# Kernel tuning notes

Hardware: AMD Instinct MI355X
Metric: run time of the kernel (lower is better)

The kernel has to match this reference:

```python
import jax, jax.numpy as jnp
import numpy as np

B, S, E, H = 4, 4096, 1024, 16
D = E // H  # head_dim = 64


def _xavier(key, out_f, in_f):
    lim = float(np.sqrt(6.0 / (in_f + out_f)))
    return jax.random.uniform(key, (out_f, in_f), jnp.float32, -lim, lim)


def setup_inputs() -> dict:
    key = jax.random.key(0)
    ks = jax.random.split(key, 9)
    x = jax.random.normal(ks[0], (B, S, E), jnp.float32)
    Wq = _xavier(ks[1], E, E)
    Wk = _xavier(ks[2], E, E)
    Wv = _xavier(ks[3], E, E)
    Wo = _xavier(ks[4], E, E)
    bq = jnp.zeros((E,), jnp.float32)
    bk = jnp.zeros((E,), jnp.float32)
    bv = jnp.zeros((E,), jnp.float32)
    bo = jnp.zeros((E,), jnp.float32)
    return {"x": x, "Wq": Wq, "bq": bq, "Wk": Wk, "bk": bk,
            "Wv": Wv, "bv": bv, "Wo": Wo, "bo": bo}


def _feature_map(t):
    # elu(t) + 1 (positive feature map)
    return jax.nn.elu(t) + 1.0


def reference(x, Wq, bq, Wk, bk, Wv, bv, Wo, bo):
    b, s, _ = x.shape
    # projections (torch Linear: y = x @ W.T + b), reshape to [b, s, h, d]
    Q = (x @ Wq.T + bq).reshape(b, s, H, D)
    K = (x @ Wk.T + bk).reshape(b, s, H, D)
    V = (x @ Wv.T + bv).reshape(b, s, H, D)
    Q = _feature_map(Q)
    K = _feature_map(K)
    # KV summary: [b, h, d, e]
    KV = jnp.einsum('bshd,bshe->bhde', K, V)
    K_sum = K.sum(axis=1)  # [b, h, d]
    Z = 1.0 / (jnp.einsum('bshd,bhd->bsh', Q, K_sum) + 1e-6)  # [b, s, h]
    out = jnp.einsum('bshd,bhde,bsh->bshe', Q, KV, Z)  # [b, s, h, e]
    out = out.reshape(b, s, E)
    out = out @ Wo.T + bo
    return out
```

## Files before the change

### kernel.cpp

```cpp
#include <hip/hip_runtime.h>
#include <math.h>

#define BB 4
#define SS 4096
#define EE 1024
#define HH 16
#define DD 64
#define MM (BB*SS)

typedef _Float16 f16x8 __attribute__((ext_vector_type(8)));
typedef _Float16 f16x4 __attribute__((ext_vector_type(4)));
typedef float    f32x4 __attribute__((ext_vector_type(4)));

typedef __attribute__((address_space(3))) void lds_void;
typedef __attribute__((address_space(1))) void gm_void;

__device__ __forceinline__ void gload16(const void* g, void* l) {
  __builtin_amdgcn_global_load_lds((gm_void*)g, (lds_void*)l, 16, 0, 0);
}

__global__ __launch_bounds__(256) void conv_all_kernel(const float* __restrict__ x,
                                                       const float* __restrict__ Wq,
                                                       const float* __restrict__ Wk,
                                                       const float* __restrict__ Wv,
                                                       const float* __restrict__ Wo,
                                                       _Float16* __restrict__ xh,
                                                       _Float16* __restrict__ wqkv,
                                                       _Float16* __restrict__ woh) {
  const int nx4 = (MM * EE) / 4;
  const int per = (EE * EE) / 4;
  const int ntot = nx4 + 4 * per;
  int i = blockIdx.x * blockDim.x + threadIdx.x;
  int stride = gridDim.x * blockDim.x;
  for (; i < ntot; i += stride) {
    const float* src;
    _Float16* dst;
    int off;
    if (i < nx4) {
      src = x; dst = xh; off = i;
    } else {
      int j = i - nx4;
      int seg = j / per; off = j - seg * per;
      src = (seg == 0) ? Wq : (seg == 1) ? Wk : (seg == 2) ? Wv : Wo;
      dst = (seg < 3) ? (wqkv + (size_t)seg * EE * EE) : woh;
    }
    f32x4 v = *(const f32x4*)&src[(size_t)off * 4];
    f16x4 h;
    h[0] = (_Float16)v[0]; h[1] = (_Float16)v[1];
    h[2] = (_Float16)v[2]; h[3] = (_Float16)v[3];
    *(f16x4*)&dst[(size_t)off * 4] = h;
  }
}


#define SCB() __builtin_amdgcn_sched_barrier(0)
#define VMW0 asm volatile("s_waitcnt vmcnt(0)" ::: "memory")
#define BARR do { SCB(); __builtin_amdgcn_s_barrier(); SCB(); } while (0)

#define STAGE_A(t, g) gload16(Ag + ((size_t)(g) << 15) + (size_t)(t) * 64,   \
                              LdsA + (((t) & 1) << 14) + (((wv << 2) + (g)) << 10))
#define STAGE_B(t, g) gload16(Bg + ((size_t)(g) << 15) + (size_t)(t) * 64,   \
                              LdsB + (((t) & 1) << 13) + (((wv << 1) + (g)) << 10))
#define STG6(t) do { STAGE_A(t, 0); STAGE_A(t, 1); STAGE_A(t, 2);            \
                     STAGE_B(t, 0); STAGE_B(t, 1); STAGE_A(t, 3); } while (0)

#define RD_A(par, mf) (*(const f16x8*)(LdsA + ((par) << 14) + ((wr8 + (mf)) << 10) + lof))
#define RD_B(par, nf) (*(const f16x8*)(LdsB + ((par) << 13) + ((wc4 + (nf)) << 10) + lof))

template <int EPI>
__global__ __launch_bounds__(256, 3) void gemm256(const _Float16* __restrict__ A,
                                                  const _Float16* __restrict__ Bw,
                                                  const float* __restrict__ bias0,
                                                  const float* __restrict__ bias1,
                                                  const float* __restrict__ bias2,
                                                  _Float16* __restrict__ O0,
                                                  _Float16* __restrict__ O1,
                                                  _Float16* __restrict__ O2,
                                                  float* __restrict__ OF) {
  __shared__ __align__(16) char lds[49152];
  char* LdsA = lds;
  char* LdsB = lds + 32768;

  const int tid  = threadIdx.x;
  const int lane = tid & 63;
  const int wv   = tid >> 6;
  const int wr   = wv >> 1;
  const int wc   = wv & 1;
  const int wr8  = wr << 3;
  const int wc4  = wc << 2;

  constexpr int NXT = (EPI == 0) ? 24 : 8;
  const int q = (int)gridDim.x >> 3;
  const int bid = (int)blockIdx.x;
  const int sid = (bid & 7) * q + (bid >> 3);
  const int mbase = (sid / NXT) << 8;
  const int nbase = (sid % NXT) << 7;

  const int lof = ((lane & 15) << 6) + (((lane >> 4) ^ ((lane >> 1) & 3)) << 4);
  const int plane = ((lane >> 2) << 11) + (((lane & 3) ^ ((lane >> 3) & 3)) << 4);

  const char* Ag = (const char*)A + ((size_t)(mbase + (wv << 6)) << 11) + plane;
  const char* Bg = (const char*)Bw + ((size_t)(nbase + (wv << 5)) << 11) + plane;

  f32x4 acc[8][4] = {};

  STG6(0);
  VMW0; BARR;

#pragma unroll 1
  for (int t = 0; t < 32; ++t) {
    const int par = t & 1;
    if (t < 31) STG6(t + 1);
    f16x8 fB0 = RD_B(par, 0), fB1 = RD_B(par, 1);
    f16x8 fB2 = RD_B(par, 2), fB3 = RD_B(par, 3);
    __builtin_amdgcn_s_setprio(1);
#pragma unroll
    for (int mf = 0; mf < 8; mf++) {
      if (mf == 4) SCB();
      f16x8 fA = RD_A(par, mf);
      acc[mf][0] = __builtin_amdgcn_mfma_f32_16x16x32_f16(fA, fB0, acc[mf][0], 0, 0, 0);
      acc[mf][1] = __builtin_amdgcn_mfma_f32_16x16x32_f16(fA, fB1, acc[mf][1], 0, 0, 0);
      acc[mf][2] = __builtin_amdgcn_mfma_f32_16x16x32_f16(fA, fB2, acc[mf][2], 0, 0, 0);
      acc[mf][3] = __builtin_amdgcn_mfma_f32_16x16x32_f16(fA, fB3, acc[mf][3], 0, 0, 0);
    }
    __builtin_amdgcn_s_setprio(0);
    if (t < 31) { VMW0; BARR; }
  }

  const int rl = (lane >> 4) << 2;
  const int cl = lane & 15;
  const int rb = mbase + (wr << 7);
  if (EPI == 0) {
    const int which = nbase >> 10;
    const float* bias = (which == 0) ? bias0 : (which == 1) ? bias1 : bias2;
    _Float16* O = (which == 0) ? O0 : (which == 1) ? O1 : O2;
    const int cb = (nbase & 1023) + (wc << 6);
#pragma unroll
    for (int mf = 0; mf < 8; mf++) {
      const int gm = rb + (mf << 4) + rl;
#pragma unroll
      for (int nf = 0; nf < 4; nf++) {
        const int gc = cb + (nf << 4) + cl;
        const float bz = bias[gc];
#pragma unroll
        for (int j = 0; j < 4; j++) {
          float v = acc[mf][nf][j] + bz;
          if (which < 2) v = (v > 0.f) ? (v + 1.f) : expf(v);
          O[(size_t)(gm + j) * EE + gc] = (_Float16)v;
        }
      }
    }
  } else {
    const int cb = nbase + (wc << 6);
#pragma unroll
    for (int mf = 0; mf < 8; mf++) {
      const int gm = rb + (mf << 4) + rl;
#pragma unroll
      for (int nf = 0; nf < 4; nf++) {
        const int gc = cb + (nf << 4) + cl;
        const float bz = bias0[gc];
#pragma unroll
        for (int j = 0; j < 4; j++)
          OF[(size_t)(gm + j) * EE + gc] = acc[mf][nf][j] + bz;
      }
    }
  }
}

#undef RD_A
#undef RD_B
#undef STG6
#undef STAGE_A
#undef STAGE_B

__global__ __launch_bounds__(256) void kv_partial_kernel(const _Float16* __restrict__ Kh,
                                                         const _Float16* __restrict__ Vh,
                                                         float* __restrict__ kvpart,
                                                         float* __restrict__ ksump) {
  __shared__ __align__(16) _Float16 Ks[64 * 64];
  __shared__ __align__(16) _Float16 Vs[64 * 64];
  const int tid = threadIdx.x;
  const int wv = tid >> 6;
  const int bh = blockIdx.x;
  const int chunk = blockIdx.y;
  const int b = bh >> 4, h = bh & 15;
  const int td = tid >> 4, te = tid & 15;
  const int d0 = td * 4, e0 = te * 4;

  float kv[4][4] = {};
  float ks4[4] = {0.f, 0.f, 0.f, 0.f};

  for (int sub = 0; sub < 4; sub++) {
    const int s0 = chunk * 256 + sub * 64;
    __syncthreads();
    {
      const int g0 = tid, g1 = tid + 256;
      gload16((const char*)Kh + ((size_t)(b * SS + s0 + (g0 >> 3)) * EE + h * DD) * 2 + (g0 & 7) * 16,
              (char*)Ks + wv * 1024);
      gload16((const char*)Kh + ((size_t)(b * SS + s0 + (g1 >> 3)) * EE + h * DD) * 2 + (g1 & 7) * 16,
              (char*)Ks + 4096 + wv * 1024);
      gload16((const char*)Vh + ((size_t)(b * SS + s0 + (g0 >> 3)) * EE + h * DD) * 2 + (g0 & 7) * 16,
              (char*)Vs + wv * 1024);
      gload16((const char*)Vh + ((size_t)(b * SS + s0 + (g1 >> 3)) * EE + h * DD) * 2 + (g1 & 7) * 16,
              (char*)Vs + 4096 + wv * 1024);
    }
    __syncthreads();
#pragma unroll 8
    for (int s = 0; s < 64; s++) {
      f16x4 kk = *(const f16x4*)&Ks[s * 64 + d0];
      f16x4 vv = *(const f16x4*)&Vs[s * 64 + e0];
      float kf[4], vf[4];
#pragma unroll
      for (int i = 0; i < 4; i++) { kf[i] = (float)kk[i]; vf[i] = (float)vv[i]; }
#pragma unroll
      for (int i = 0; i < 4; i++)
#pragma unroll
        for (int j = 0; j < 4; j++) kv[i][j] += kf[i] * vf[j];
      if (te == 0) {
#pragma unroll
        for (int i = 0; i < 4; i++) ks4[i] += kf[i];
      }
    }
  }
  const size_t base = ((size_t)chunk * 64 + bh) * 4096;
#pragma unroll
  for (int i = 0; i < 4; i++)
#pragma unroll
    for (int j = 0; j < 4; j++) kvpart[base + (size_t)(d0 + i) * 64 + e0 + j] = kv[i][j];
  if (te == 0) {
#pragma unroll
    for (int i = 0; i < 4; i++) ksump[((size_t)chunk * 64 + bh) * 64 + d0 + i] = ks4[i];
  }
}

__global__ __launch_bounds__(256) void kv_reduce_kernel(const float* __restrict__ kvpart,
                                                        const float* __restrict__ ksump,
                                                        _Float16* __restrict__ kvt,
                                                        float* __restrict__ ksum) {
  const int idx = blockIdx.x * 256 + threadIdx.x;
  if (blockIdx.x < 1024) {
    const int bh = idx >> 12;
    const int rem = idx & 4095;
    float s = 0.f;
#pragma unroll
    for (int c = 0; c < 16; c++) s += kvpart[((size_t)c * 64 + bh) * 4096 + rem];
    const int d = rem >> 6, e = rem & 63;
    kvt[(size_t)bh * 4096 + e * 64 + d] = (_Float16)s;
  } else {
    const int i2 = idx - 1024 * 256;
    const int bh = i2 >> 6, d = i2 & 63;
    float s = 0.f;
#pragma unroll
    for (int c = 0; c < 16; c++) s += ksump[((size_t)c * 64 + bh) * 64 + d];
    ksum[i2] = s;
  }
}

__global__ __launch_bounds__(256) void attn_kernel(const _Float16* __restrict__ Qh,
                                                   const _Float16* __restrict__ kvt,
                                                   const float* __restrict__ ksum,
                                                   _Float16* __restrict__ attn) {
  __shared__ __align__(16) _Float16 Qs[64 * 64];
  __shared__ __align__(16) _Float16 KVs[64 * 64];
  __shared__ float ks_lds[64];
  __shared__ float dpart[4][64];
  __shared__ float zr[64];
  const int tid = threadIdx.x;
  const int lane = tid & 63;
  const int wv = tid >> 6;
  const int stile = blockIdx.x;
  const int bh = blockIdx.y;
  const int b = bh >> 4, h = bh & 15;
  const int m0 = b * SS + stile * 64;

  {
    const int g0 = tid, g1 = tid + 256;
    gload16((const char*)Qh + ((size_t)(m0 + (g0 >> 3)) * EE + h * DD) * 2 + (g0 & 7) * 16,
            (char*)Qs + wv * 1024);
    gload16((const char*)Qh + ((size_t)(m0 + (g1 >> 3)) * EE + h * DD) * 2 + (g1 & 7) * 16,
            (char*)Qs + 4096 + wv * 1024);
    gload16((const char*)kvt + (size_t)bh * 8192 + (size_t)g0 * 16, (char*)KVs + wv * 1024);
    gload16((const char*)kvt + (size_t)bh * 8192 + (size_t)g1 * 16, (char*)KVs + 4096 + wv * 1024);
  }
  if (tid < 64) ks_lds[tid] = ksum[bh * 64 + tid];
  __syncthreads();

  {
    const int r = tid & 63, qd = tid >> 6;
    float p = 0.f;
#pragma unroll
    for (int i = 0; i < 16; i++) p += (float)Qs[r * 64 + qd * 16 + i] * ks_lds[qd * 16 + i];
    dpart[qd][r] = p;
  }
  __syncthreads();
  if (tid < 64) {
    float den = dpart[0][tid] + dpart[1][tid] + dpart[2][tid] + dpart[3][tid];
    zr[tid] = 1.f / (den + 1e-6f);
  }
  __syncthreads();

  f32x4 acc[4] = {};
  const int fr = lane & 15;
  const int kg = (lane >> 4) * 8;
#pragma unroll
  for (int kh = 0; kh < 2; kh++) {
    f16x8 a = *(const f16x8*)&Qs[(wv * 16 + fr) * 64 + kh * 32 + kg];
#pragma unroll
    for (int n = 0; n < 4; n++) {
      f16x8 b8 = *(const f16x8*)&KVs[(n * 16 + fr) * 64 + kh * 32 + kg];
      acc[n] = __builtin_amdgcn_mfma_f32_16x16x32_f16(a, b8, acc[n], 0, 0, 0);
    }
  }

  const int rl = (lane >> 4) * 4, cl = lane & 15;
#pragma unroll
  for (int n = 0; n < 4; n++)
#pragma unroll
    for (int j = 0; j < 4; j++) {
      const int r = wv * 16 + rl + j;
      float v = acc[n][j] * zr[r];
      attn[(size_t)(m0 + r) * EE + h * DD + n * 16 + cl] = (_Float16)v;
    }
}

extern "C" void kernel_launch(void* const* d_in, const int* in_sizes, int n_in,
                              void* d_out, int out_size, void* d_ws, size_t ws_size,
                              hipStream_t stream) {
  const float* x  = (const float*)d_in[0];
  const float* Wq = (const float*)d_in[1];
  const float* bq = (const float*)d_in[2];
  const float* Wk = (const float*)d_in[3];
  const float* bk = (const float*)d_in[4];
  const float* Wv = (const float*)d_in[5];
  const float* bv = (const float*)d_in[6];
  const float* Wo = (const float*)d_in[7];
  const float* bo = (const float*)d_in[8];
  float* out = (float*)d_out;

  char* ws = (char*)d_ws;
  size_t off = 0;
  auto alloc = [&](size_t bytes) -> char* {
    char* p = ws + off;
    off += (bytes + 255) & ~(size_t)255;
    return p;
  };
  _Float16* xh    = (_Float16*)alloc((size_t)MM * EE * 2);
  _Float16* wqkv  = (_Float16*)alloc((size_t)3 * EE * EE * 2);
  _Float16* woh   = (_Float16*)alloc((size_t)EE * EE * 2);
  _Float16* Qh    = (_Float16*)alloc((size_t)MM * EE * 2);
  _Float16* Kh    = (_Float16*)alloc((size_t)MM * EE * 2);
  _Float16* Vh    = (_Float16*)alloc((size_t)MM * EE * 2);
  float*    kvpart= (float*)alloc((size_t)16 * 64 * 4096 * 4);
  float*    ksump = (float*)alloc((size_t)16 * 64 * 64 * 4);
  _Float16* kvt   = (_Float16*)alloc((size_t)64 * 4096 * 2);
  float*    ksum  = (float*)alloc((size_t)64 * 64 * 4);
  _Float16* attn  = xh;

  (void)in_sizes; (void)n_in; (void)out_size; (void)ws_size;

  conv_all_kernel<<<2560, 256, 0, stream>>>(x, Wq, Wk, Wv, Wo, xh, wqkv, woh);
  gemm256<0><<<1536, 256, 0, stream>>>(xh, wqkv, bq, bk, bv, Qh, Kh, Vh, nullptr);
  kv_partial_kernel<<<dim3(64, 16), 256, 0, stream>>>(Kh, Vh, kvpart, ksump);
  kv_reduce_kernel<<<1040, 256, 0, stream>>>(kvpart, ksump, kvt, ksum);
  attn_kernel<<<dim3(64, 64), 256, 0, stream>>>(Qh, kvt, ksum, attn);
  gemm256<1><<<512, 256, 0, stream>>>(attn, woh, bo, nullptr, nullptr,
                                      nullptr, nullptr, nullptr, out);
}
```

Measured before the change: 261.8 us.

## Triple-buffer GEMM LDS staging with two tiles in flight

Changes the GEMM main loop from double to triple buffering in LDS. Two k-tiles are now prefetched, and each step waits with vmcnt(6) so only the older tile has to land, which hides more global-load latency. The loop is unrolled by three so buffer indices are compile-time constants. LDS grows from 48KB to 72KB and the occupancy hint drops from 3 to 2 blocks per CU, trading occupancy for deeper prefetch.

```diff
diff --git a/kernel.cpp b/kernel.cpp
--- a/kernel.cpp
+++ b/kernel.cpp
@@ -54,21 +54,40 @@
 
 
 #define SCB() __builtin_amdgcn_sched_barrier(0)
+#define VMW6 asm volatile("s_waitcnt vmcnt(6)" ::: "memory")
 #define VMW0 asm volatile("s_waitcnt vmcnt(0)" ::: "memory")
 #define BARR do { SCB(); __builtin_amdgcn_s_barrier(); SCB(); } while (0)
-
-#define STAGE_A(t, g) gload16(Ag + ((size_t)(g) << 15) + (size_t)(t) * 64,   \
-                              LdsA + (((t) & 1) << 14) + (((wv << 2) + (g)) << 10))
-#define STAGE_B(t, g) gload16(Bg + ((size_t)(g) << 15) + (size_t)(t) * 64,   \
-                              LdsB + (((t) & 1) << 13) + (((wv << 1) + (g)) << 10))
-#define STG6(t) do { STAGE_A(t, 0); STAGE_A(t, 1); STAGE_A(t, 2);            \
-                     STAGE_B(t, 0); STAGE_B(t, 1); STAGE_A(t, 3); } while (0)
-
-#define RD_A(par, mf) (*(const f16x8*)(LdsA + ((par) << 14) + ((wr8 + (mf)) << 10) + lof))
-#define RD_B(par, nf) (*(const f16x8*)(LdsB + ((par) << 13) + ((wc4 + (nf)) << 10) + lof))
+#define NOP_ do {} while (0)
+
+#define STAGE_A(t, g, bf) gload16(Ag + ((size_t)(g) << 15) + (size_t)(t) * 64, \
+                                  LdsA + (bf) * 16384 + (((wv << 2) + (g)) << 10))
+#define STAGE_B(t, g, bf) gload16(Bg + ((size_t)(g) << 15) + (size_t)(t) * 64, \
+                                  LdsB + (bf) * 8192 + (((wv << 1) + (g)) << 10))
+#define STG6(t, bf) do { STAGE_A(t, 0, bf); STAGE_A(t, 1, bf); STAGE_A(t, 2, bf); \
+                         STAGE_B(t, 0, bf); STAGE_B(t, 1, bf); STAGE_A(t, 3, bf); } while (0)
+
+#define RD_A(bf, mf) (*(const f16x8*)(LdsA + (bf) * 16384 + ((wr8 + (mf)) << 10) + lof))
+#define RD_B(bf, nf) (*(const f16x8*)(LdsB + (bf) * 8192 + ((wc4 + (nf)) << 10) + lof))
+
+#define TILE_(bf, STG, VW, BAR) do {                                         \
+    STG;                                                                     \
+    f16x8 fB0 = RD_B(bf, 0), fB1 = RD_B(bf, 1);                              \
+    f16x8 fB2 = RD_B(bf, 2), fB3 = RD_B(bf, 3);                              \
+    __builtin_amdgcn_s_setprio(1);                                           \
+    _Pragma("unroll") for (int mf = 0; mf < 8; mf++) {                       \
+      if (mf == 4) SCB();                                                    \
+      f16x8 fA = RD_A(bf, mf);                                               \
+      acc[mf][0] = __builtin_amdgcn_mfma_f32_16x16x32_f16(fA, fB0, acc[mf][0], 0, 0, 0); \
+      acc[mf][1] = __builtin_amdgcn_mfma_f32_16x16x32_f16(fA, fB1, acc[mf][1], 0, 0, 0); \
+      acc[mf][2] = __builtin_amdgcn_mfma_f32_16x16x32_f16(fA, fB2, acc[mf][2], 0, 0, 0); \
+      acc[mf][3] = __builtin_amdgcn_mfma_f32_16x16x32_f16(fA, fB3, acc[mf][3], 0, 0, 0); \
+    }                                                                        \
+    __builtin_amdgcn_s_setprio(0);                                           \
+    VW; BAR;                                                                 \
+  } while (0)
 
 template <int EPI>
-__global__ __launch_bounds__(256, 3) void gemm256(const _Float16* __restrict__ A,
+__global__ __launch_bounds__(256, 2) void gemm256(const _Float16* __restrict__ A,
                                                   const _Float16* __restrict__ Bw,
                                                   const float* __restrict__ bias0,
                                                   const float* __restrict__ bias1,
@@ -77,9 +96,9 @@
                                                   _Float16* __restrict__ O1,
                                                   _Float16* __restrict__ O2,
                                                   float* __restrict__ OF) {
-  __shared__ __align__(16) char lds[49152];
+  __shared__ __align__(16) char lds[73728];
   char* LdsA = lds;
-  char* LdsB = lds + 32768;
+  char* LdsB = lds + 49152;
 
   const int tid  = threadIdx.x;
   const int lane = tid & 63;
@@ -104,28 +123,18 @@
 
   f32x4 acc[8][4] = {};
 
-  STG6(0);
-  VMW0; BARR;
+  STG6(0, 0); STG6(1, 1);
+  VMW6; BARR;
 
 #pragma unroll 1
-  for (int t = 0; t < 32; ++t) {
-    const int par = t & 1;
-    if (t < 31) STG6(t + 1);
-    f16x8 fB0 = RD_B(par, 0), fB1 = RD_B(par, 1);
-    f16x8 fB2 = RD_B(par, 2), fB3 = RD_B(par, 3);
-    __builtin_amdgcn_s_setprio(1);
-#pragma unroll
-    for (int mf = 0; mf < 8; mf++) {
-      if (mf == 4) SCB();
-      f16x8 fA = RD_A(par, mf);
-      acc[mf][0] = __builtin_amdgcn_mfma_f32_16x16x32_f16(fA, fB0, acc[mf][0], 0, 0, 0);
-      acc[mf][1] = __builtin_amdgcn_mfma_f32_16x16x32_f16(fA, fB1, acc[mf][1], 0, 0, 0);
-      acc[mf][2] = __builtin_amdgcn_mfma_f32_16x16x32_f16(fA, fB2, acc[mf][2], 0, 0, 0);
-      acc[mf][3] = __builtin_amdgcn_mfma_f32_16x16x32_f16(fA, fB3, acc[mf][3], 0, 0, 0);
-    }
-    __builtin_amdgcn_s_setprio(0);
-    if (t < 31) { VMW0; BARR; }
-  }
+  for (int i = 0; i < 10; ++i) {
+    const int t = i * 3;
+    TILE_(0, STG6(t + 2, 2), VMW6, BARR);
+    TILE_(1, STG6(t + 3, 0), VMW6, BARR);
+    TILE_(2, STG6(t + 4, 1), VMW6, BARR);
+  }
+  TILE_(0, NOP_, VMW0, BARR);
+  TILE_(1, NOP_, NOP_, NOP_);
 
   const int rl = (lane >> 4) << 2;
   const int cl = lane & 15;
@@ -167,6 +176,7 @@
   }
 }
 
+#undef TILE_
 #undef RD_A
 #undef RD_B
 #undef STG6
```

Measured after the change: 265.1 us. Within noise of the previous version (+1.3%).

## Rework GEMM to 256x256 tiles with 8 waves and phased k-pipelining

Applied to the files above, without the earlier changes.

The GEMM kernel moves from 256x128 tiles with 4 waves and K-step 32 to 256x256 tiles with 8 waves, K-step 64 and a 128KB double-buffered LDS. Each K tile is split into four phases that interleave global-to-LDS prefetch of future tiles with MFMA work, using partial vmcnt waits instead of a full drain. The intent is higher arithmetic intensity per tile, fewer barrier stalls and better overlap of loads with compute. In exchange the kernel uses much more LDS per block, which lowers occupancy, and the barrier schedule is more complex.

```diff
diff --git a/kernel.cpp b/kernel.cpp
--- a/kernel.cpp
+++ b/kernel.cpp
@@ -53,22 +53,59 @@
 }
 
 
-#define SCB() __builtin_amdgcn_sched_barrier(0)
+#define VMW6 asm volatile("s_waitcnt vmcnt(6)" ::: "memory")
 #define VMW0 asm volatile("s_waitcnt vmcnt(0)" ::: "memory")
-#define BARR do { SCB(); __builtin_amdgcn_s_barrier(); SCB(); } while (0)
-
-#define STAGE_A(t, g) gload16(Ag + ((size_t)(g) << 15) + (size_t)(t) * 64,   \
-                              LdsA + (((t) & 1) << 14) + (((wv << 2) + (g)) << 10))
-#define STAGE_B(t, g) gload16(Bg + ((size_t)(g) << 15) + (size_t)(t) * 64,   \
-                              LdsB + (((t) & 1) << 13) + (((wv << 1) + (g)) << 10))
-#define STG6(t) do { STAGE_A(t, 0); STAGE_A(t, 1); STAGE_A(t, 2);            \
-                     STAGE_B(t, 0); STAGE_B(t, 1); STAGE_A(t, 3); } while (0)
-
-#define RD_A(par, mf) (*(const f16x8*)(LdsA + ((par) << 14) + ((wr8 + (mf)) << 10) + lof))
-#define RD_B(par, nf) (*(const f16x8*)(LdsB + ((par) << 13) + ((wc4 + (nf)) << 10) + lof))
+#define NOP_ do {} while (0)
+
+#define STA(t, h) do {                                                        \
+    const char* s_ = AgL + (size_t)(h) * 262144 + (size_t)(t) * 128;          \
+    char* d_ = LdsA + (((t) & 1) << 15) + ((h) << 14) + (wv << 10);           \
+    gload16(s_, d_); gload16(s_ + 131072, d_ + 8192);                         \
+  } while (0)
+#define STB(t, h) do {                                                        \
+    const char* s_ = BgL + (size_t)(h) * 262144 + (size_t)(t) * 128;          \
+    char* d_ = LdsB + (((t) & 1) << 15) + ((h) << 14) + (wv << 10);           \
+    gload16(s_, d_); gload16(s_ + 131072, d_ + 8192);                         \
+  } while (0)
+
+#define RA(bu, mf, ks) (*(const f16x8*)(LdsA + ((bu) << 15) + (wr << 14) +    \
+    ((mf) << 11) + frb + ((ks) ? so1 : so0)))
+#define RB(bu, nf, ks) (*(const f16x8*)(LdsB + ((bu) << 15) + ((wc >> 1) << 14) + \
+    ((((wc & 1) << 2) | (nf)) << 11) + frb + ((ks) ? so1 : so0)))
+
+#define PHASE(t, P, STG, VMC) do {                                            \
+    const int bu = (t) & 1;                                                   \
+    if ((P) == 0) {                                                           \
+      _Pragma("unroll") for (int nf = 0; nf < 4; nf++) {                      \
+        bfr[nf][0] = RB(bu, nf, 0); bfr[nf][1] = RB(bu, nf, 1);               \
+      }                                                                       \
+    }                                                                         \
+    f16x8 a00 = RA(bu, 2 * (P), 0),     a01 = RA(bu, 2 * (P), 1);             \
+    f16x8 a10 = RA(bu, 2 * (P) + 1, 0), a11 = RA(bu, 2 * (P) + 1, 1);         \
+    STG;                                                                      \
+    __builtin_amdgcn_s_barrier();                                             \
+    __builtin_amdgcn_s_setprio(1);                                            \
+    _Pragma("unroll") for (int nf = 0; nf < 4; nf++) {                        \
+      acc[2*(P)][nf]   = __builtin_amdgcn_mfma_f32_16x16x32_f16(a00, bfr[nf][0], acc[2*(P)][nf], 0, 0, 0);   \
+      acc[2*(P)][nf]   = __builtin_amdgcn_mfma_f32_16x16x32_f16(a01, bfr[nf][1], acc[2*(P)][nf], 0, 0, 0);   \
+      acc[2*(P)+1][nf] = __builtin_amdgcn_mfma_f32_16x16x32_f16(a10, bfr[nf][0], acc[2*(P)+1][nf], 0, 0, 0); \
+      acc[2*(P)+1][nf] = __builtin_amdgcn_mfma_f32_16x16x32_f16(a11, bfr[nf][1], acc[2*(P)+1][nf], 0, 0, 0); \
+    }                                                                         \
+    __builtin_amdgcn_s_setprio(0);                                            \
+    VMC;                                                                      \
+    __builtin_amdgcn_s_barrier();                                             \
+  } while (0)
+
+#define TILE(t, S1, S2, S3, S4, VMC) do {                                     \
+    PHASE(t, 0, S1, NOP_);                                                    \
+    PHASE(t, 1, S2, NOP_);                                                    \
+    PHASE(t, 2, S3, NOP_);                                                    \
+    PHASE(t, 3, S4, VMC);                                                     \
+    __builtin_amdgcn_sched_barrier(0);                                        \
+  } while (0)
 
 template <int EPI>
-__global__ __launch_bounds__(256, 3) void gemm256(const _Float16* __restrict__ A,
+__global__ __launch_bounds__(512, 2) void gemm256(const _Float16* __restrict__ A,
                                                   const _Float16* __restrict__ Bw,
                                                   const float* __restrict__ bias0,
                                                   const float* __restrict__ bias1,
@@ -77,55 +114,52 @@
                                                   _Float16* __restrict__ O1,
                                                   _Float16* __restrict__ O2,
                                                   float* __restrict__ OF) {
-  __shared__ __align__(16) char lds[49152];
+  __shared__ __align__(16) char lds[131072];
   char* LdsA = lds;
-  char* LdsB = lds + 32768;
+  char* LdsB = lds + 65536;
 
   const int tid  = threadIdx.x;
   const int lane = tid & 63;
   const int wv   = tid >> 6;
-  const int wr   = wv >> 1;
-  const int wc   = wv & 1;
-  const int wr8  = wr << 3;
-  const int wc4  = wc << 2;
-
-  constexpr int NXT = (EPI == 0) ? 24 : 8;
+  const int wr   = wv >> 2;
+  const int wc   = wv & 3;
+
+  constexpr int NX = (EPI == 0) ? 12 : 4;
   const int q = (int)gridDim.x >> 3;
   const int bid = (int)blockIdx.x;
   const int sid = (bid & 7) * q + (bid >> 3);
-  const int mbase = (sid / NXT) << 8;
-  const int nbase = (sid % NXT) << 7;
-
-  const int lof = ((lane & 15) << 6) + (((lane >> 4) ^ ((lane >> 1) & 3)) << 4);
-  const int plane = ((lane >> 2) << 11) + (((lane & 3) ^ ((lane >> 3) & 3)) << 4);
-
-  const char* Ag = (const char*)A + ((size_t)(mbase + (wv << 6)) << 11) + plane;
-  const char* Bg = (const char*)Bw + ((size_t)(nbase + (wv << 5)) << 11) + plane;
+  const int mbase = (sid / NX) << 8;
+  const int nbase = (sid % NX) << 8;
+
+  const int fr  = lane & 15;
+  const int kg  = lane >> 4;
+  const int frb = fr << 7;
+  const int so0 = ((kg ^ (fr & 7)) << 4);
+  const int so1 = (((4 | kg) ^ (fr & 7)) << 4);
+  const int srcsl = (((lane & 7) ^ (lane >> 3)) << 4);
+
+  const char* AgL = (const char*)A +
+      ((size_t)(mbase + (wv << 3) + (lane >> 3)) << 11) + srcsl;
+  const char* BgL = (const char*)Bw +
+      ((size_t)(nbase + (wv << 3) + (lane >> 3)) << 11) + srcsl;
 
   f32x4 acc[8][4] = {};
-
-  STG6(0);
-  VMW0; BARR;
+  f16x8 bfr[4][2];
+
+  STA(0, 0); STA(0, 1); STB(0, 0); STB(0, 1);
+  STB(1, 0); STB(1, 1); STA(1, 0);
+  VMW6;
+  __builtin_amdgcn_s_barrier();
+  __builtin_amdgcn_sched_barrier(0);
 
 #pragma unroll 1
-  for (int t = 0; t < 32; ++t) {
-    const int par = t & 1;
-    if (t < 31) STG6(t + 1);
-    f16x8 fB0 = RD_B(par, 0), fB1 = RD_B(par, 1);
-    f16x8 fB2 = RD_B(par, 2), fB3 = RD_B(par, 3);
-    __builtin_amdgcn_s_setprio(1);
-#pragma unroll
-    for (int mf = 0; mf < 8; mf++) {
-      if (mf == 4) SCB();
-      f16x8 fA = RD_A(par, mf);
-      acc[mf][0] = __builtin_amdgcn_mfma_f32_16x16x32_f16(fA, fB0, acc[mf][0], 0, 0, 0);
-      acc[mf][1] = __builtin_amdgcn_mfma_f32_16x16x32_f16(fA, fB1, acc[mf][1], 0, 0, 0);
-      acc[mf][2] = __builtin_amdgcn_mfma_f32_16x16x32_f16(fA, fB2, acc[mf][2], 0, 0, 0);
-      acc[mf][3] = __builtin_amdgcn_mfma_f32_16x16x32_f16(fA, fB3, acc[mf][3], 0, 0, 0);
-    }
-    __builtin_amdgcn_s_setprio(0);
-    if (t < 31) { VMW0; BARR; }
-  }
+  for (int i = 0; i < 7; ++i) {
+    const int t = i << 1;
+    TILE(t,     STA(t + 1, 1), STB(t + 2, 0), STB(t + 2, 1), STA(t + 2, 0), VMW6);
+    TILE(t + 1, STA(t + 2, 1), STB(t + 3, 0), STB(t + 3, 1), STA(t + 3, 0), VMW6);
+  }
+  TILE(14, STA(15, 1), NOP_, NOP_, NOP_, VMW0);
+  TILE(15, NOP_, NOP_, NOP_, NOP_, NOP_);
 
   const int rl = (lane >> 4) << 2;
   const int cl = lane & 15;
@@ -167,11 +201,12 @@
   }
 }
 
-#undef RD_A
-#undef RD_B
-#undef STG6
-#undef STAGE_A
-#undef STAGE_B
+#undef TILE
+#undef PHASE
+#undef RA
+#undef RB
+#undef STA
+#undef STB
 
 __global__ __launch_bounds__(256) void kv_partial_kernel(const _Float16* __restrict__ Kh,
                                                          const _Float16* __restrict__ Vh,
@@ -359,10 +394,10 @@
   (void)in_sizes; (void)n_in; (void)out_size; (void)ws_size;
 
   conv_all_kernel<<<2560, 256, 0, stream>>>(x, Wq, Wk, Wv, Wo, xh, wqkv, woh);
-  gemm256<0><<<1536, 256, 0, stream>>>(xh, wqkv, bq, bk, bv, Qh, Kh, Vh, nullptr);
+  gemm256<0><<<768, 512, 0, stream>>>(xh, wqkv, bq, bk, bv, Qh, Kh, Vh, nullptr);
   kv_partial_kernel<<<dim3(64, 16), 256, 0, stream>>>(Kh, Vh, kvpart, ksump);
   kv_reduce_kernel<<<1040, 256, 0, stream>>>(kvpart, ksump, kvt, ksum);
   attn_kernel<<<dim3(64, 64), 256, 0, stream>>>(Qh, kvt, ksum, attn);
-  gemm256<1><<<512, 256, 0, stream>>>(attn, woh, bo, nullptr, nullptr,
+  gemm256<1><<<256, 512, 0, stream>>>(attn, woh, bo, nullptr, nullptr,
                                       nullptr, nullptr, nullptr, out);
 }
```

Measured after the change: 255.3 us. 2.5% less time.
